# Kernel tuning notes

Hardware: AMD Instinct MI355X
Metric: run time of the kernel (lower is better)

## Reference

```python
import jax, jax.numpy as jnp
import numpy as np

DIM = 128
H = 8
HD = DIM // H
NL = 6
DFF = 2048
EPS = 1e-5
S2S_STEPS = 6


def _ln(x, g, b):
    m = jnp.mean(x, -1, keepdims=True)
    v = jnp.mean(jnp.square(x - m), -1, keepdims=True)
    return (x - m) / jnp.sqrt(v + EPS) * g + b


def _lstm_step(x, h, c, wih, whh, bih, bhh):
    # torch LSTM gate order: i, f, g, o
    gates = x @ wih.T + bih + h @ whh.T + bhh
    i, f, g, o = jnp.split(gates, 4, axis=-1)
    c = jax.nn.sigmoid(f) * c + jax.nn.sigmoid(i) * jnp.tanh(g)
    h = jax.nn.sigmoid(o) * jnp.tanh(c)
    return h, c


def setup_inputs() -> dict:
    key = jax.random.key(0)
    ks = iter(jax.random.split(key, 16))
    n = lambda shape: jax.random.normal(next(ks), shape, jnp.float32) * 0.02
    inp = {
        "data": jax.random.normal(next(ks), (64, 256, 3), jnp.float32),
        "lin0_w": n((DIM, 3)), "lin0_b": jnp.zeros((DIM,), jnp.float32),
        "attn_in_w": n((NL, 3 * DIM, DIM)), "attn_in_b": jnp.zeros((NL, 3 * DIM), jnp.float32),
        "attn_out_w": n((NL, DIM, DIM)), "attn_out_b": jnp.zeros((NL, DIM), jnp.float32),
        "ln1_g": jnp.ones((NL, DIM), jnp.float32), "ln1_b": jnp.zeros((NL, DIM), jnp.float32),
        "ff_w1": n((NL, DFF, DIM)), "ff_b1": jnp.zeros((NL, DFF), jnp.float32),
        "ff_w2": n((NL, DIM, DFF)), "ff_b2": jnp.zeros((NL, DIM), jnp.float32),
        "ln2_g": jnp.ones((NL, DIM), jnp.float32), "ln2_b": jnp.zeros((NL, DIM), jnp.float32),
        "s2s_wih": n((4 * DIM, 2 * DIM)), "s2s_whh": n((4 * DIM, DIM)),
        "s2s_bih": jnp.zeros((4 * DIM,), jnp.float32), "s2s_bhh": jnp.zeros((4 * DIM,), jnp.float32),
        "mem_wih": n((4 * DIM, 2 * DIM)), "mem_whh": n((4 * DIM, DIM)),
        "mem_bih": jnp.zeros((4 * DIM,), jnp.float32), "mem_bhh": jnp.zeros((4 * DIM,), jnp.float32),
        "lin1_w": n((DIM, DIM)), "lin1_b": jnp.zeros((DIM,), jnp.float32),
        "lin3_w": n((1, DIM)), "lin3_b": jnp.zeros((1,), jnp.float32),
    }
    return inp


def reference(data, lin0_w, lin0_b, attn_in_w, attn_in_b, attn_out_w, attn_out_b,
              ln1_g, ln1_b, ff_w1, ff_b1, ff_w2, ff_b2, ln2_g, ln2_b,
              s2s_wih, s2s_whh, s2s_bih, s2s_bhh,
              mem_wih, mem_whh, mem_bih, mem_bhh,
              lin1_w, lin1_b, lin3_w, lin3_b):
    x = jax.nn.relu(data @ lin0_w.T + lin0_b)  # [S=64, B=256, D]
    S, B, _ = x.shape
    # torch TransformerEncoder with batch_first=False: attention over axis 0,
    # axis 1 is the transformer batch. Post-norm layers (norm_first=False), relu FFN.
    for l in range(NL):
        qkv = x @ attn_in_w[l].T + attn_in_b[l]
        q, k, v = jnp.split(qkv, 3, axis=-1)
        q = q.reshape(S, B, H, HD)
        k = k.reshape(S, B, H, HD)
        v = v.reshape(S, B, H, HD)
        scores = jnp.einsum('sbhd,tbhd->bhst', q, k) / np.float32(np.sqrt(HD))
        attn = jax.nn.softmax(scores, axis=-1)
        ao = jnp.einsum('bhst,tbhd->sbhd', attn, v).reshape(S, B, DIM)
        x = _ln(x + ao @ attn_out_w[l].T + attn_out_b[l], ln1_g[l], ln1_b[l])
        ff = jax.nn.relu(x @ ff_w1[l].T + ff_b1[l]) @ ff_w2[l].T + ff_b2[l]
        x = _ln(x + ff, ln2_g[l], ln2_b[l])
    # Set2Set pooling: bidxs assign segment = axis-0 index for each block of
    # num_atoms consecutive rows of flatten(out,0,1), i.e. pool over axis 1.
    q_star = jnp.zeros((S, 2 * DIM), x.dtype)
    h = jnp.zeros((S, DIM), x.dtype)
    c = jnp.zeros((S, DIM), x.dtype)
    for _ in range(S2S_STEPS):
        h, c = _lstm_step(q_star, h, c, s2s_wih, s2s_whh, s2s_bih, s2s_bhh)
        e = jnp.einsum('bnd,bd->bn', x, h)          # [S, num_atoms]
        a = jax.nn.softmax(e, axis=-1)              # segment softmax (uniform segs)
        r = jnp.einsum('bn,bnd->bd', a, x)          # segment weighted sum
        q_star = jnp.concatenate([h, r], axis=-1)   # [S, 2D]
    # memory LSTM: seq_len 1, zero initial state (states=None branch)
    hx = jnp.zeros((S, DIM), x.dtype)
    cx = jnp.zeros((S, DIM), x.dtype)
    hx, cx = _lstm_step(q_star, hx, cx, mem_wih, mem_whh, mem_bih, mem_bhh)
    o = jax.nn.relu(hx @ lin1_w.T + lin1_b)
    v_out = (o @ lin3_w.T + lin3_b)[None]  # [1, S, 1]
    return v_out, hx[None], cx[None]
```

## Files before the change

kernel.cpp:

```cpp
#include <hip/hip_runtime.h>
#include <math.h>


typedef _Float16 __attribute__((ext_vector_type(8))) f16x8;
typedef __attribute__((ext_vector_type(4))) float f32x4;
typedef _Float16 __attribute__((ext_vector_type(2))) h16x2;

__device__ __forceinline__ unsigned short f2h(float f) {
  union { _Float16 h; unsigned short s; } x; x.h = (_Float16)f; return x.s;
}
__device__ __forceinline__ float h2f(unsigned short u) {
  union { unsigned short s; _Float16 h; } x; x.s = u; return (float)x.h;
}
__device__ __forceinline__ unsigned packh(float a, float b) {
  return (unsigned)f2h(a) | ((unsigned)f2h(b) << 16);
}
__device__ __forceinline__ uint2 pk4(float a, float b, float c, float d) {
  return make_uint2(packh(a, b), packh(c, d));
}
__device__ __forceinline__ float hlo(unsigned u) {
  union { unsigned short s; _Float16 h; } x; x.s = (unsigned short)(u & 0xffff);
  return (float)x.h;
}
__device__ __forceinline__ float hhi(unsigned u) {
  union { unsigned short s; _Float16 h; } x; x.s = (unsigned short)(u >> 16);
  return (float)x.h;
}
__device__ __forceinline__ float fdot2u(unsigned a, unsigned b, float c) {
#if __has_builtin(__builtin_amdgcn_fdot2)
  union U { unsigned u; h16x2 h; };
  U x, y; x.u = a; y.u = b;
  return __builtin_amdgcn_fdot2(x.h, y.h, c, false);
#else
  return c + hlo(a) * hlo(b) + hhi(a) * hhi(b);
#endif
}
__device__ __forceinline__ float fexp(float x) { return __expf(x); }
__device__ __forceinline__ float sigf(float x) {
  return 1.f / (1.f + __expf(-x));
}
__device__ __forceinline__ float ftanh(float x) {
  float e = __expf(2.f * x);
  return 1.f - 2.f / (e + 1.f);
}

__device__ __forceinline__ void gl2lds16(const void* g, void* l) {
  __builtin_amdgcn_global_load_lds(
      (const __attribute__((address_space(1))) unsigned int*)g,
      (__attribute__((address_space(3))) unsigned int*)l, 16, 0, 0);
}

__global__ __launch_bounds__(256) void convw_kernel(
    const float* __restrict__ aiw, const float* __restrict__ aow,
    const float* __restrict__ w1, const float* __restrict__ w2,
    const float* __restrict__ wih, const float* __restrict__ whh,
    const float* __restrict__ mwih,
    unsigned short* __restrict__ o0, unsigned short* __restrict__ o1,
    unsigned short* __restrict__ o2, unsigned short* __restrict__ o3,
    unsigned short* __restrict__ o4, unsigned short* __restrict__ o5,
    unsigned short* __restrict__ o6) {
  int i = blockIdx.x * 256 + threadIdx.x;
  if (i < 294912) {
    int l = i / 49152, o = i % 49152;
    int j = o & 7, fr = (o >> 3) & 15, fq = (o >> 7) & 3, ks = (o >> 9) & 3,
        rb = o >> 11;
    o0[i] = f2h(aiw[l * 49152 + (rb * 16 + fr) * 128 + ks * 32 + fq * 8 + j]);
  } else if (i < 393216) {
    int ii = i - 294912;
    int l = ii / 16384, o = ii % 16384;
    int j = o & 7, fr = (o >> 3) & 15, fq = (o >> 7) & 3, ks = (o >> 9) & 3,
        rb = o >> 11;
    o1[ii] = f2h(aow[l * 16384 + (rb * 16 + fr) * 128 + ks * 32 + fq * 8 + j]);
  } else if (i < 1966080) {
    int ii = i - 393216;
    int l = ii >> 18, o = ii & 262143;
    int j = o & 7, fr = (o >> 3) & 15, fq = (o >> 7) & 3, ks = (o >> 9) & 3,
        rb = o >> 11;
    o2[ii] = f2h(w1[l * 262144 + (rb * 16 + fr) * 128 + ks * 32 + fq * 8 + j]);
  } else if (i < 3538944) {
    int ii = i - 1966080;
    int l = ii >> 18, o = ii & 262143;
    int j = o & 7, fr = (o >> 3) & 15, fq = (o >> 7) & 3, ks = (o >> 9) & 63,
        rb = o >> 15;
    o3[ii] = f2h(w2[l * 262144 + (rb * 16 + fr) * 2048 + ks * 32 + fq * 8 + j]);
  } else if (i < 3670016) {
    int j = i - 3538944; o4[j] = f2h(wih[j]);
  } else if (i < 3735552) {
    int j = i - 3670016; o5[j] = f2h(whh[j]);
  } else {
    int j = i - 3735552; o6[j] = f2h(mwih[j]);
  }
}

__global__ __launch_bounds__(256) void lin0_kernel(
    const float* __restrict__ data, const float* __restrict__ w,
    const float* __restrict__ b, float* __restrict__ x,
    unsigned short* __restrict__ xb) {
  int i = blockIdx.x * 256 + threadIdx.x;
  int n = i >> 7, d = i & 127;
  float v = b[d] + data[n * 3 + 0] * w[d * 3 + 0]
                 + data[n * 3 + 1] * w[d * 3 + 1]
                 + data[n * 3 + 2] * w[d * 3 + 2];
  v = fmaxf(v, 0.0f);
  x[i] = v;
  xb[i] = f2h(v);
}

__global__ __launch_bounds__(256, 2) void layer_kernel(
    const unsigned short* __restrict__ xbg,
    const unsigned short* __restrict__ wqkv, const float* __restrict__ bqkv,
    const unsigned short* __restrict__ wout, const float* __restrict__ bout,
    const float* __restrict__ ln1g, const float* __restrict__ ln1b,
    const unsigned short* __restrict__ w1, const float* __restrict__ b1,
    const unsigned short* __restrict__ w2, const float* __restrict__ b2,
    const float* __restrict__ ln2g, const float* __restrict__ ln2b,
    float* __restrict__ xio, unsigned short* __restrict__ xbo) {
  __shared__ __align__(16) unsigned short SM[28672];
  __shared__ float psum[4][32], psq[4][32];
  __shared__ float2 stats[32];
  __shared__ __align__(16) uint4 zchunk;

  unsigned short* Xs = SM;
  unsigned short* Ks = SM + 8192;
  unsigned short* VT = SM + 16384;
  unsigned short* AOs = SM + 16384;
  unsigned short* Qs = SM + 24576;
  unsigned short* Xn = SM + 24576;

  int tid = threadIdx.x, w = tid >> 6, lane = tid & 63;
  int b = blockIdx.x >> 1, half = blockIdx.x & 1;
  int r4 = lane >> 4, cs = lane & 15;
  int fr = lane & 15, fq = lane >> 4;

  if (tid == 0) zchunk = make_uint4(0u, 0u, 0u, 0u);

#pragma unroll
  for (int i = 0; i < 4; i++) {
    int issue = w * 4 + i;
    int row = issue * 4 + r4;
    int g = cs ^ (row & 7);
    gl2lds16(xbg + (size_t)(row * 256 + b) * 128 + g * 8,
             (char*)Xs + issue * 1024);
  }
  f16x8 wq[4][2];
#pragma unroll
  for (int ks = 0; ks < 4; ks++)
#pragma unroll
    for (int ni = 0; ni < 2; ni++)
      wq[ks][ni] = *(const f16x8*)(wqkv + (size_t)(w * 2 + ni) * 2048 +
                                   ks * 512 + fq * 128 + fr * 8);
  __syncthreads();

  {
    f32x4 acc[2][2];
#pragma unroll
    for (int i = 0; i < 2; i++)
#pragma unroll
      for (int j = 0; j < 2; j++) acc[i][j] = (f32x4){0.f, 0.f, 0.f, 0.f};
#pragma unroll
    for (int ks = 0; ks < 4; ks++) {
      f16x8 bx[2];
#pragma unroll
      for (int mi2 = 0; mi2 < 2; mi2++) {
        int row = half * 32 + mi2 * 16 + fr;
        int kq = (ks * 4 + fq) ^ (row & 7);
        bx[mi2] = *(const f16x8*)(Xs + row * 128 + kq * 8);
      }
#pragma unroll
      for (int mi2 = 0; mi2 < 2; mi2++)
#pragma unroll
        for (int ni = 0; ni < 2; ni++)
          acc[mi2][ni] = __builtin_amdgcn_mfma_f32_16x16x32_f16(
              wq[ks][ni], bx[mi2], acc[mi2][ni], 0, 0, 0);
    }
#pragma unroll
    for (int ni = 0; ni < 2; ni++) {
      int fb = (w * 2 + ni) * 16 + fq * 4;
      float4 bv = *(const float4*)&bqkv[fb];
#pragma unroll
      for (int mi2 = 0; mi2 < 2; mi2++) {
        int srow = mi2 * 16 + fr;
        *(uint2*)(Qs + srow * 128 + (((fb >> 3) ^ (srow & 7)) << 3) +
                  (fb & 7)) =
            pk4(acc[mi2][ni][0] + bv.x, acc[mi2][ni][1] + bv.y,
                acc[mi2][ni][2] + bv.z, acc[mi2][ni][3] + bv.w);
      }
    }
  }
  {
    f16x8 wk[4][2];
#pragma unroll
    for (int ks = 0; ks < 4; ks++)
#pragma unroll
      for (int ni = 0; ni < 2; ni++)
        wk[ks][ni] = *(const f16x8*)(wqkv + (size_t)(8 + w * 2 + ni) * 2048 +
                                     ks * 512 + fq * 128 + fr * 8);
    f32x4 acc[4][2];
#pragma unroll
    for (int i = 0; i < 4; i++)
#pragma unroll
      for (int j = 0; j < 2; j++) acc[i][j] = (f32x4){0.f, 0.f, 0.f, 0.f};
#pragma unroll
    for (int ks = 0; ks < 4; ks++) {
      f16x8 bx[4];
#pragma unroll
      for (int mi = 0; mi < 4; mi++) {
        int row = mi * 16 + fr;
        int kq = (ks * 4 + fq) ^ (row & 7);
        bx[mi] = *(const f16x8*)(Xs + row * 128 + kq * 8);
      }
#pragma unroll
      for (int mi = 0; mi < 4; mi++)
#pragma unroll
        for (int ni = 0; ni < 2; ni++)
          acc[mi][ni] = __builtin_amdgcn_mfma_f32_16x16x32_f16(
              wk[ks][ni], bx[mi], acc[mi][ni], 0, 0, 0);
    }
#pragma unroll
    for (int ni = 0; ni < 2; ni++) {
      int fb = (w * 2 + ni) * 16 + fq * 4;
      float4 bv = *(const float4*)&bqkv[128 + fb];
#pragma unroll
      for (int mi = 0; mi < 4; mi++) {
        int srow = mi * 16 + fr;
        *(uint2*)(Ks + srow * 128 + (((fb >> 3) ^ (srow & 7)) << 3) +
                  (fb & 7)) =
            pk4(acc[mi][ni][0] + bv.x, acc[mi][ni][1] + bv.y,
                acc[mi][ni][2] + bv.z, acc[mi][ni][3] + bv.w);
      }
    }
  }
  {
    f16x8 wv[4][2];
#pragma unroll
    for (int ks = 0; ks < 4; ks++)
#pragma unroll
      for (int ni = 0; ni < 2; ni++)
        wv[ks][ni] = *(const f16x8*)(wqkv + (size_t)(16 + w * 2 + ni) * 2048 +
                                     ks * 512 + fq * 128 + fr * 8);
    f32x4 acc[4][2];
#pragma unroll
    for (int i = 0; i < 4; i++)
#pragma unroll
      for (int j = 0; j < 2; j++) acc[i][j] = (f32x4){0.f, 0.f, 0.f, 0.f};
#pragma unroll
    for (int ks = 0; ks < 4; ks++) {
      f16x8 ax[4];
#pragma unroll
      for (int mi = 0; mi < 4; mi++) {
        int row = mi * 16 + fr;
        int kq = (ks * 4 + fq) ^ (row & 7);
        ax[mi] = *(const f16x8*)(Xs + row * 128 + kq * 8);
      }
#pragma unroll
      for (int mi = 0; mi < 4; mi++)
#pragma unroll
        for (int ni = 0; ni < 2; ni++)
          acc[mi][ni] = __builtin_amdgcn_mfma_f32_16x16x32_f16(
              ax[mi], wv[ks][ni], acc[mi][ni], 0, 0, 0);
    }
#pragma unroll
    for (int ni = 0; ni < 2; ni++) {
      int feat = (w * 2 + ni) * 16 + fr;
      float bv = bqkv[256 + feat];
#pragma unroll
      for (int mi = 0; mi < 4; mi++) {
        int sb = mi * 16 + fq * 4;
        *(uint2*)(VT + feat * 64 + (((sb >> 3) ^ (feat & 7)) << 3) +
                  (sb & 7)) =
            pk4(acc[mi][ni][0] + bv, acc[mi][ni][1] + bv,
                acc[mi][ni][2] + bv, acc[mi][ni][3] + bv);
      }
    }
  }
  f16x8 wo[4][2];
#pragma unroll
  for (int ks = 0; ks < 4; ks++)
#pragma unroll
    for (int ni = 0; ni < 2; ni++)
      wo[ks][ni] = *(const f16x8*)(wout + (size_t)(w * 2 + ni) * 2048 +
                                   ks * 512 + fq * 128 + fr * 8);
  __syncthreads();

  f32x4 po[2][2];
#pragma unroll
  for (int i = 0; i < 2; i++)
#pragma unroll
    for (int j = 0; j < 2; j++) po[i][j] = (f32x4){0.f, 0.f, 0.f, 0.f};
  {
    unsigned short* Pb = Xs + w * 2048;
#pragma unroll
    for (int hi = 0; hi < 2; hi++) {
      int h = w * 2 + hi;
      f16x8 afH[2], bfH[4];
#pragma unroll
      for (int mi2 = 0; mi2 < 2; mi2++) {
        int qrow = mi2 * 16 + fr;
        const unsigned short* pa =
            (fq < 2) ? (Qs + qrow * 128 + (((h * 2 + fq) ^ (qrow & 7)) << 3))
                     : (const unsigned short*)&zchunk;
        afH[mi2] = *(const f16x8*)pa;
      }
#pragma unroll
      for (int ti = 0; ti < 4; ti++) {
        int trow = ti * 16 + fr;
        const unsigned short* pb =
            (fq < 2) ? (Ks + trow * 128 + (((h * 2 + fq) ^ (trow & 7)) << 3))
                     : (const unsigned short*)&zchunk;
        bfH[ti] = *(const f16x8*)pb;
      }
      f32x4 sc[2][4];
#pragma unroll
      for (int i = 0; i < 2; i++)
#pragma unroll
        for (int j = 0; j < 4; j++) sc[i][j] = (f32x4){0.f, 0.f, 0.f, 0.f};
#pragma unroll
      for (int mi2 = 0; mi2 < 2; mi2++)
#pragma unroll
        for (int ti = 0; ti < 4; ti++)
          sc[mi2][ti] = __builtin_amdgcn_mfma_f32_16x16x32_f16(
              afH[mi2], bfH[ti], sc[mi2][ti], 0, 0, 0);
#pragma unroll
      for (int mi2 = 0; mi2 < 2; mi2++) {
#pragma unroll
        for (int r = 0; r < 4; r++) {
          float m = -1e30f;
#pragma unroll
          for (int ti = 0; ti < 4; ti++) m = fmaxf(m, sc[mi2][ti][r]);
          m = fmaxf(m, __shfl_xor(m, 1, 64));
          m = fmaxf(m, __shfl_xor(m, 2, 64));
          m = fmaxf(m, __shfl_xor(m, 4, 64));
          m = fmaxf(m, __shfl_xor(m, 8, 64));
          m *= 0.25f;
          float ss = 0.f;
#pragma unroll
          for (int ti = 0; ti < 4; ti++) {
            float p = fexp(sc[mi2][ti][r] * 0.25f - m);
            sc[mi2][ti][r] = p;
            ss += p;
          }
          ss += __shfl_xor(ss, 1, 64);
          ss += __shfl_xor(ss, 2, 64);
          ss += __shfl_xor(ss, 4, 64);
          ss += __shfl_xor(ss, 8, 64);
          float inv = 1.f / ss;
          int prow = mi2 * 16 + fq * 4 + r;
#pragma unroll
          for (int ti = 0; ti < 4; ti++) {
            int t = ti * 16 + fr;
            Pb[prow * 64 + (((t >> 3) ^ (prow & 7)) << 3) + (t & 7)] =
                f2h(sc[mi2][ti][r] * inv);
          }
        }
      }
#pragma unroll
      for (int ks2 = 0; ks2 < 2; ks2++) {
        f16x8 bp[2], avt;
#pragma unroll
        for (int si2 = 0; si2 < 2; si2++) {
          int prow = si2 * 16 + fr;
          int kq = (ks2 * 4 + fq) ^ (prow & 7);
          bp[si2] = *(const f16x8*)(Pb + prow * 64 + kq * 8);
        }
        {
          int vrow = h * 16 + fr;
          int kq = (ks2 * 4 + fq) ^ (vrow & 7);
          avt = *(const f16x8*)(VT + vrow * 64 + kq * 8);
        }
#pragma unroll
        for (int si2 = 0; si2 < 2; si2++)
          po[hi][si2] = __builtin_amdgcn_mfma_f32_16x16x32_f16(
              avt, bp[si2], po[hi][si2], 0, 0, 0);
      }
    }
  }
  __syncthreads();
#pragma unroll
  for (int hi = 0; hi < 2; hi++) {
    int fb = (w * 2 + hi) * 16 + fq * 4;
#pragma unroll
    for (int si2 = 0; si2 < 2; si2++) {
      int srow = si2 * 16 + fr;
      *(uint2*)(AOs + srow * 128 + (((fb >> 3) ^ (srow & 7)) << 3) +
                (fb & 7)) =
          pk4(po[hi][si2][0], po[hi][si2][1], po[hi][si2][2], po[hi][si2][3]);
    }
  }
  __syncthreads();

  {
    f32x4 acc[2][2];
#pragma unroll
    for (int i = 0; i < 2; i++)
#pragma unroll
      for (int j = 0; j < 2; j++) acc[i][j] = (f32x4){0.f, 0.f, 0.f, 0.f};
#pragma unroll
    for (int ks = 0; ks < 4; ks++) {
      f16x8 bao[2];
#pragma unroll
      for (int mi2 = 0; mi2 < 2; mi2++) {
        int row = mi2 * 16 + fr;
        int kq = (ks * 4 + fq) ^ (row & 7);
        bao[mi2] = *(const f16x8*)(AOs + row * 128 + kq * 8);
      }
#pragma unroll
      for (int mi2 = 0; mi2 < 2; mi2++)
#pragma unroll
        for (int ni = 0; ni < 2; ni++)
          acc[mi2][ni] = __builtin_amdgcn_mfma_f32_16x16x32_f16(
              wo[ks][ni], bao[mi2], acc[mi2][ni], 0, 0, 0);
    }
    float v4[2][2][4];
    float psA[2] = {0.f, 0.f}, psQ[2] = {0.f, 0.f};
#pragma unroll
    for (int ni = 0; ni < 2; ni++) {
      int fb = (w * 2 + ni) * 16 + fq * 4;
      float4 bv = *(const float4*)&bout[fb];
#pragma unroll
      for (int mi2 = 0; mi2 < 2; mi2++) {
        int rowg = half * 32 + mi2 * 16 + fr;
        float4 rs = *(const float4*)&xio[(size_t)(rowg * 256 + b) * 128 + fb];
        float t0 = acc[mi2][ni][0] + bv.x + rs.x;
        float t1 = acc[mi2][ni][1] + bv.y + rs.y;
        float t2 = acc[mi2][ni][2] + bv.z + rs.z;
        float t3 = acc[mi2][ni][3] + bv.w + rs.w;
        v4[ni][mi2][0] = t0; v4[ni][mi2][1] = t1;
        v4[ni][mi2][2] = t2; v4[ni][mi2][3] = t3;
        psA[mi2] += (t0 + t1) + (t2 + t3);
        psQ[mi2] += (t0 * t0 + t1 * t1) + (t2 * t2 + t3 * t3);
      }
    }
#pragma unroll
    for (int mi2 = 0; mi2 < 2; mi2++) {
      psA[mi2] += __shfl_xor(psA[mi2], 16, 64);
      psA[mi2] += __shfl_xor(psA[mi2], 32, 64);
      psQ[mi2] += __shfl_xor(psQ[mi2], 16, 64);
      psQ[mi2] += __shfl_xor(psQ[mi2], 32, 64);
    }
    if (fq == 0) {
#pragma unroll
      for (int mi2 = 0; mi2 < 2; mi2++) {
        psum[w][mi2 * 16 + fr] = psA[mi2];
        psq[w][mi2 * 16 + fr] = psQ[mi2];
      }
    }
    __syncthreads();
    if (tid < 32) {
      float S = 0.f, Q = 0.f;
#pragma unroll
      for (int ww = 0; ww < 4; ww++) { S += psum[ww][tid]; Q += psq[ww][tid]; }
      float m = S * (1.f / 128.f);
      float var = Q * (1.f / 128.f) - m * m;
      stats[tid] = make_float2(m, rsqrtf(var + 1e-5f));
    }
    __syncthreads();
#pragma unroll
    for (int ni = 0; ni < 2; ni++) {
      int fb = (w * 2 + ni) * 16 + fq * 4;
      float4 g4 = *(const float4*)&ln1g[fb];
      float4 b4 = *(const float4*)&ln1b[fb];
#pragma unroll
      for (int mi2 = 0; mi2 < 2; mi2++) {
        int srow = mi2 * 16 + fr;
        float2 st = stats[srow];
        float y0 = (v4[ni][mi2][0] - st.x) * st.y * g4.x + b4.x;
        float y1 = (v4[ni][mi2][1] - st.x) * st.y * g4.y + b4.y;
        float y2 = (v4[ni][mi2][2] - st.x) * st.y * g4.z + b4.z;
        float y3 = (v4[ni][mi2][3] - st.x) * st.y * g4.w + b4.w;
        *(uint2*)(Xn + srow * 128 + (((fb >> 3) ^ (srow & 7)) << 3) +
                  (fb & 7)) = pk4(y0, y1, y2, y3);
      }
    }
  }
  __syncthreads();

  f16x8 xfragF[4][2];
#pragma unroll
  for (int ks = 0; ks < 4; ks++)
#pragma unroll
    for (int mi2 = 0; mi2 < 2; mi2++) {
      int rowl = mi2 * 16 + fr;
      int kq = (ks * 4 + fq) ^ (rowl & 7);
      xfragF[ks][mi2] = *(const f16x8*)(Xn + rowl * 128 + kq * 8);
    }

  f32x4 acc2[2][2];
#pragma unroll
  for (int i = 0; i < 2; i++)
#pragma unroll
    for (int j = 0; j < 2; j++) acc2[i][j] = (f32x4){0.f, 0.f, 0.f, 0.f};

  for (int c = 0; c < 8; c++) {
    unsigned short* Hcur = SM + (c & 1) * 8192;
    f16x8 aw1[4][4];
#pragma unroll
    for (int ks = 0; ks < 4; ks++)
#pragma unroll
      for (int ni = 0; ni < 4; ni++)
        aw1[ks][ni] = *(const f16x8*)(w1 + (size_t)(c * 16 + w * 4 + ni) *
                                              2048 +
                                      ks * 512 + fq * 128 + fr * 8);
    f32x4 acc1[2][4];
#pragma unroll
    for (int i = 0; i < 2; i++)
#pragma unroll
      for (int j = 0; j < 4; j++) acc1[i][j] = (f32x4){0.f, 0.f, 0.f, 0.f};
#pragma unroll
    for (int ks = 0; ks < 4; ks++)
#pragma unroll
      for (int mi2 = 0; mi2 < 2; mi2++)
#pragma unroll
        for (int ni = 0; ni < 4; ni++)
          acc1[mi2][ni] = __builtin_amdgcn_mfma_f32_16x16x32_f16(
              aw1[ks][ni], xfragF[ks][mi2], acc1[mi2][ni], 0, 0, 0);
#pragma unroll
    for (int ni = 0; ni < 4; ni++) {
      int hb = (w * 4 + ni) * 16 + fq * 4;
      float4 bv = *(const float4*)&b1[c * 256 + hb];
#pragma unroll
      for (int mi2 = 0; mi2 < 2; mi2++) {
        int srow = mi2 * 16 + fr;
        *(uint2*)(Hcur + srow * 256 + (((hb >> 3) ^ (srow & 7)) << 3) +
                  (hb & 7)) =
            pk4(fmaxf(acc1[mi2][ni][0] + bv.x, 0.f),
                fmaxf(acc1[mi2][ni][1] + bv.y, 0.f),
                fmaxf(acc1[mi2][ni][2] + bv.z, 0.f),
                fmaxf(acc1[mi2][ni][3] + bv.w, 0.f));
      }
    }
    f16x8 aw2[8][2];
#pragma unroll
    for (int ks2 = 0; ks2 < 8; ks2++)
#pragma unroll
      for (int ni = 0; ni < 2; ni++)
        aw2[ks2][ni] = *(const f16x8*)(w2 + (size_t)(w * 2 + ni) * 32768 +
                                       (c * 8 + ks2) * 512 + fq * 128 +
                                       fr * 8);
    __syncthreads();
#pragma unroll
    for (int ks2 = 0; ks2 < 8; ks2++) {
      f16x8 bh[2];
#pragma unroll
      for (int mi2 = 0; mi2 < 2; mi2++) {
        int row = mi2 * 16 + fr;
        int kq = (ks2 * 4 + fq) ^ (row & 7);
        bh[mi2] = *(const f16x8*)(Hcur + row * 256 + kq * 8);
      }
#pragma unroll
      for (int mi2 = 0; mi2 < 2; mi2++)
#pragma unroll
        for (int ni = 0; ni < 2; ni++)
          acc2[mi2][ni] = __builtin_amdgcn_mfma_f32_16x16x32_f16(
              aw2[ks2][ni], bh[mi2], acc2[mi2][ni], 0, 0, 0);
    }
  }

  {
    float v4[2][2][4];
    float psA[2] = {0.f, 0.f}, psQ[2] = {0.f, 0.f};
#pragma unroll
    for (int ni = 0; ni < 2; ni++) {
      int fb = (w * 2 + ni) * 16 + fq * 4;
      float4 bv = *(const float4*)&b2[fb];
#pragma unroll
      for (int mi2 = 0; mi2 < 2; mi2++) {
        int srow = mi2 * 16 + fr;
        uint2 rz = *(const uint2*)(Xn + srow * 128 +
                                   (((fb >> 3) ^ (srow & 7)) << 3) + (fb & 7));
        float t0 = acc2[mi2][ni][0] + bv.x + hlo(rz.x);
        float t1 = acc2[mi2][ni][1] + bv.y + hhi(rz.x);
        float t2 = acc2[mi2][ni][2] + bv.z + hlo(rz.y);
        float t3 = acc2[mi2][ni][3] + bv.w + hhi(rz.y);
        v4[ni][mi2][0] = t0; v4[ni][mi2][1] = t1;
        v4[ni][mi2][2] = t2; v4[ni][mi2][3] = t3;
        psA[mi2] += (t0 + t1) + (t2 + t3);
        psQ[mi2] += (t0 * t0 + t1 * t1) + (t2 * t2 + t3 * t3);
      }
    }
#pragma unroll
    for (int mi2 = 0; mi2 < 2; mi2++) {
      psA[mi2] += __shfl_xor(psA[mi2], 16, 64);
      psA[mi2] += __shfl_xor(psA[mi2], 32, 64);
      psQ[mi2] += __shfl_xor(psQ[mi2], 16, 64);
      psQ[mi2] += __shfl_xor(psQ[mi2], 32, 64);
    }
    if (fq == 0) {
#pragma unroll
      for (int mi2 = 0; mi2 < 2; mi2++) {
        psum[w][mi2 * 16 + fr] = psA[mi2];
        psq[w][mi2 * 16 + fr] = psQ[mi2];
      }
    }
    __syncthreads();
    if (tid < 32) {
      float S = 0.f, Q = 0.f;
#pragma unroll
      for (int ww = 0; ww < 4; ww++) { S += psum[ww][tid]; Q += psq[ww][tid]; }
      float m = S * (1.f / 128.f);
      float var = Q * (1.f / 128.f) - m * m;
      stats[tid] = make_float2(m, rsqrtf(var + 1e-5f));
    }
    __syncthreads();
#pragma unroll
    for (int ni = 0; ni < 2; ni++) {
      int fb = (w * 2 + ni) * 16 + fq * 4;
      float4 g4 = *(const float4*)&ln2g[fb];
      float4 b4 = *(const float4*)&ln2b[fb];
#pragma unroll
      for (int mi2 = 0; mi2 < 2; mi2++) {
        int srow = mi2 * 16 + fr;
        float2 st = stats[srow];
        float y0 = (v4[ni][mi2][0] - st.x) * st.y * g4.x + b4.x;
        float y1 = (v4[ni][mi2][1] - st.x) * st.y * g4.y + b4.y;
        float y2 = (v4[ni][mi2][2] - st.x) * st.y * g4.z + b4.z;
        float y3 = (v4[ni][mi2][3] - st.x) * st.y * g4.w + b4.w;
        size_t o = (size_t)((half * 32 + srow) * 256 + b) * 128 + fb;
        *(float4*)&xio[o] = make_float4(y0, y1, y2, y3);
        *(uint2*)&xbo[o] = pk4(y0, y1, y2, y3);
      }
    }
  }
}

__global__ __launch_bounds__(512, 1) void s2s_kernel(
    const unsigned short* __restrict__ xb,
    const unsigned short* __restrict__ wihh,
    const unsigned short* __restrict__ whhh,
    const float* __restrict__ bih, const float* __restrict__ bhh,
    const unsigned short* __restrict__ mwihh,
    const float* __restrict__ mbih, const float* __restrict__ mbhh,
    const float* __restrict__ l1w, const float* __restrict__ l1b,
    const float* __restrict__ l3w, const float* __restrict__ l3b,
    float* __restrict__ out) {
  __shared__ __align__(16) unsigned xl[256 * 65];
  __shared__ __align__(16) unsigned qu[128];
  __shared__ __align__(16) float cst[128];
  __shared__ __align__(16) float gates[512];
  __shared__ __align__(16) float red[256];
  __shared__ __align__(16) float aw[256];
  int s = blockIdx.x, t = threadIdx.x, lane = t & 63, w = t >> 6;

  uint4 wreg[32], ureg[16];
  {
    const uint4* wp = (const uint4*)(wihh + (size_t)t * 256);
#pragma unroll
    for (int i = 0; i < 32; i++) wreg[i] = wp[i];
    const uint4* up = (const uint4*)(whhh + (size_t)t * 128);
#pragma unroll
    for (int i = 0; i < 16; i++) ureg[i] = up[i];
  }

  const uint4* xs4 = (const uint4*)(xb + (size_t)s * 32768);
#pragma unroll
  for (int it = 0; it < 8; it++) {
    int f = it * 512 + t;
    uint4 v = xs4[f];
    int n = f >> 4, jc = (f & 15) * 4;
    unsigned* dst = xl + n * 65 + jc;
    dst[0] = v.x; dst[1] = v.y; dst[2] = v.z; dst[3] = v.w;
  }
  if (t < 128) cst[t] = 0.f;
  __syncthreads();

  const uint4* q4 = (const uint4*)qu;
  float bsum = bih[t] + bhh[t];

  for (int step = 0; step < 6; step++) {
    if (step > 0) {
      float a0 = 0.f, a1 = 0.f, a2 = 0.f, a3 = 0.f;
#pragma unroll
      for (int i = 0; i < 16; i++) {
        uint4 qv = q4[i];
        a0 = fdot2u(wreg[i].x, qv.x, a0);
        a1 = fdot2u(wreg[i].y, qv.y, a1);
        a2 = fdot2u(wreg[i].z, qv.z, a2);
        a3 = fdot2u(wreg[i].w, qv.w, a3);
        a0 = fdot2u(ureg[i].x, qv.x, a0);
        a1 = fdot2u(ureg[i].y, qv.y, a1);
        a2 = fdot2u(ureg[i].z, qv.z, a2);
        a3 = fdot2u(ureg[i].w, qv.w, a3);
      }
#pragma unroll
      for (int i = 16; i < 32; i++) {
        uint4 qv = q4[i];
        a0 = fdot2u(wreg[i].x, qv.x, a0);
        a1 = fdot2u(wreg[i].y, qv.y, a1);
        a2 = fdot2u(wreg[i].z, qv.z, a2);
        a3 = fdot2u(wreg[i].w, qv.w, a3);
      }
      gates[t] = bsum + ((a0 + a1) + (a2 + a3));
    } else {
      gates[t] = bsum;
    }
    __syncthreads();
    if (t < 128) {
      float ig = sigf(gates[t]), fg = sigf(gates[128 + t]);
      float gg = ftanh(gates[256 + t]), og = sigf(gates[384 + t]);
      float cn = fg * cst[t] + ig * gg;
      cst[t] = cn;
      float hn = og * ftanh(cn);
      float hp = __shfl_xor(hn, 1, 64);
      if ((t & 1) == 0) qu[t >> 1] = packh(hn, hp);
    }
    __syncthreads();
    if (step > 0) {
      int n = t >> 1, p = t & 1;
      const unsigned* xr = xl + n * 65 + p * 32;
      float e0 = 0.f, e1 = 0.f;
#pragma unroll 8
      for (int i = 0; i < 32; i += 2) {
        e0 = fdot2u(xr[i], qu[p * 32 + i], e0);
        e1 = fdot2u(xr[i + 1], qu[p * 32 + i + 1], e1);
      }
      float e = e0 + e1;
      e += __shfl_xor(e, 1, 64);
      if (p == 0) red[n] = e;
      __syncthreads();
      float v0 = red[lane], v1 = red[64 + lane];
      float v2 = red[128 + lane], v3 = red[192 + lane];
      float m = fmaxf(fmaxf(v0, v1), fmaxf(v2, v3));
#pragma unroll
      for (int d = 1; d < 64; d <<= 1) m = fmaxf(m, __shfl_xor(m, d, 64));
      float p0 = fexp(v0 - m), p1 = fexp(v1 - m);
      float p2 = fexp(v2 - m), p3 = fexp(v3 - m);
      float ss = p0 + p1 + p2 + p3;
#pragma unroll
      for (int d = 1; d < 64; d <<= 1) ss += __shfl_xor(ss, d, 64);
      float Sinv = 1.f / ss;
      if (w == 0) {
        aw[lane] = p0 * Sinv; aw[64 + lane] = p1 * Sinv;
        aw[128 + lane] = p2 * Sinv; aw[192 + lane] = p3 * Sinv;
      }
    } else {
      if (t < 256) aw[t] = 1.f / 256.f;
    }
    __syncthreads();
    {
      int d = t & 127, grp = t >> 7;
      const unsigned* xc = xl + grp * 64 * 65 + (d >> 1);
      int hi = d & 1;
      const float* ap = aw + grp * 64;
      float r0 = 0.f, r1 = 0.f, r2 = 0.f, r3 = 0.f;
#pragma unroll 4
      for (int n2 = 0; n2 < 64; n2 += 4) {
        unsigned u0 = xc[n2 * 65], u1 = xc[(n2 + 1) * 65];
        unsigned u2 = xc[(n2 + 2) * 65], u3 = xc[(n2 + 3) * 65];
        r0 += ap[n2] * (hi ? hhi(u0) : hlo(u0));
        r1 += ap[n2 + 1] * (hi ? hhi(u1) : hlo(u1));
        r2 += ap[n2 + 2] * (hi ? hhi(u2) : hlo(u2));
        r3 += ap[n2 + 3] * (hi ? hhi(u3) : hlo(u3));
      }
      gates[t] = (r0 + r1) + (r2 + r3);
    }
    __syncthreads();
    if (t < 128) {
      float rd = gates[t] + gates[128 + t] + gates[256 + t] + gates[384 + t];
      float rp = __shfl_xor(rd, 1, 64);
      if ((t & 1) == 0) qu[64 + (t >> 1)] = packh(rd, rp);
    }
    __syncthreads();
  }
  {
    float a0 = 0.f, a1 = 0.f, a2 = 0.f, a3 = 0.f;
    const uint4* mp = (const uint4*)(mwihh + (size_t)t * 256);
#pragma unroll 8
    for (int i = 0; i < 32; i++) {
      uint4 wv = mp[i], qv = q4[i];
      a0 = fdot2u(wv.x, qv.x, a0);
      a1 = fdot2u(wv.y, qv.y, a1);
      a2 = fdot2u(wv.z, qv.z, a2);
      a3 = fdot2u(wv.w, qv.w, a3);
    }
    gates[t] = mbih[t] + mbhh[t] + ((a0 + a1) + (a2 + a3));
  }
  __syncthreads();
  if (t < 128) {
    float ig = sigf(gates[t]);
    float gg = ftanh(gates[256 + t]);
    float og = sigf(gates[384 + t]);
    float cx = ig * gg;
    float hx = og * ftanh(cx);
    cst[t] = hx;
    out[64 + s * 128 + t] = hx;
    out[64 + 8192 + s * 128 + t] = cx;
  }
  __syncthreads();
  if (t < 128) {
    float acc = l1b[t];
    const float4* w4 = (const float4*)(l1w + (size_t)t * 128);
    const float4* h4 = (const float4*)cst;
#pragma unroll 8
    for (int k = 0; k < 32; k++) {
      float4 a = w4[k], b = h4[k];
      acc += a.x * b.x + a.y * b.y + a.z * b.z + a.w * b.w;
    }
    red[t] = fmaxf(acc, 0.f) * l3w[t];
  } else if (t < 256) {
    red[t] = 0.f;
  }
  __syncthreads();
  for (int off = 128; off; off >>= 1) {
    if (t < off) red[t] += red[t + off];
    __syncthreads();
  }
  if (t == 0) out[s] = red[0] + l3b[0];
}

extern "C" void kernel_launch(void* const* d_in, const int* in_sizes, int n_in,
                              void* d_out, int out_size, void* d_ws,
                              size_t ws_size, hipStream_t stream) {
  const float* data       = (const float*)d_in[0];
  const float* lin0_w     = (const float*)d_in[1];
  const float* lin0_b     = (const float*)d_in[2];
  const float* attn_in_w  = (const float*)d_in[3];
  const float* attn_in_b  = (const float*)d_in[4];
  const float* attn_out_w = (const float*)d_in[5];
  const float* attn_out_b = (const float*)d_in[6];
  const float* ln1_g      = (const float*)d_in[7];
  const float* ln1_b      = (const float*)d_in[8];
  const float* ff_w1      = (const float*)d_in[9];
  const float* ff_b1      = (const float*)d_in[10];
  const float* ff_w2      = (const float*)d_in[11];
  const float* ff_b2      = (const float*)d_in[12];
  const float* ln2_g      = (const float*)d_in[13];
  const float* ln2_b      = (const float*)d_in[14];
  const float* s2s_wih    = (const float*)d_in[15];
  const float* s2s_whh    = (const float*)d_in[16];
  const float* s2s_bih    = (const float*)d_in[17];
  const float* s2s_bhh    = (const float*)d_in[18];
  const float* mem_wih    = (const float*)d_in[19];
  const float* mem_bih    = (const float*)d_in[21];
  const float* mem_bhh    = (const float*)d_in[22];
  const float* lin1_w     = (const float*)d_in[23];
  const float* lin1_b     = (const float*)d_in[24];
  const float* lin3_w     = (const float*)d_in[25];
  const float* lin3_b     = (const float*)d_in[26];
  float* out = (float*)d_out;

  char* p = (char*)d_ws;
  float* x = (float*)p;                      p += (size_t)16384 * 128 * 4;
  unsigned short* xb = (unsigned short*)p;   p += (size_t)16384 * 128 * 2;
  unsigned short* wqkv = (unsigned short*)p; p += (size_t)294912 * 2;
  unsigned short* wout = (unsigned short*)p; p += (size_t)98304 * 2;
  unsigned short* w1h = (unsigned short*)p;  p += (size_t)1572864 * 2;
  unsigned short* w2h = (unsigned short*)p;  p += (size_t)1572864 * 2;
  unsigned short* wihh = (unsigned short*)p; p += (size_t)131072 * 2;
  unsigned short* whhh = (unsigned short*)p; p += (size_t)65536 * 2;
  unsigned short* mwihh = (unsigned short*)p; p += (size_t)131072 * 2;

  convw_kernel<<<15104, 256, 0, stream>>>(
      attn_in_w, attn_out_w, ff_w1, ff_w2, s2s_wih, s2s_whh, mem_wih,
      wqkv, wout, w1h, w2h, wihh, whhh, mwihh);
  lin0_kernel<<<8192, 256, 0, stream>>>(data, lin0_w, lin0_b, x, xb);

  for (int l = 0; l < 6; l++) {
    layer_kernel<<<512, 256, 0, stream>>>(
        xb, wqkv + (size_t)l * 49152, attn_in_b + l * 384,
        wout + (size_t)l * 16384, attn_out_b + l * 128,
        ln1_g + l * 128, ln1_b + l * 128,
        w1h + (size_t)l * 262144, ff_b1 + l * 2048,
        w2h + (size_t)l * 262144, ff_b2 + l * 128,
        ln2_g + l * 128, ln2_b + l * 128, x, xb);
  }

  s2s_kernel<<<64, 512, 0, stream>>>(
      xb, wihh, whhh, s2s_bih, s2s_bhh,
      mwihh, mem_bih, mem_bhh, lin1_w, lin1_b, lin3_w, lin3_b, out);
}
```

Measured before the change: 406.2 us.

## Split Set2Set LSTM work across 1024 threads and stream weights from cache

The Set2Set kernel now launches 1024 threads per block instead of 512. Each gate row's dot product is split into two halves, and the halves are summed through shared memory. The LSTM weights are no longer preloaded into registers; they are read from global memory on every step. The attention-score and weighted-sum loops are also repartitioned across the extra threads. This aims to shorten the per-step serial chain and ease register pressure, at the cost of repeated global or cache reads of the weights and extra reduction work.

```diff
diff --git a/kernel.cpp b/kernel.cpp
--- a/kernel.cpp
+++ b/kernel.cpp
@@ -622,7 +622,7 @@
   }
 }
 
-__global__ __launch_bounds__(512, 1) void s2s_kernel(
+__global__ __launch_bounds__(1024, 1) void s2s_kernel(
     const unsigned short* __restrict__ xb,
     const unsigned short* __restrict__ wihh,
     const unsigned short* __restrict__ whhh,
@@ -635,25 +635,16 @@
   __shared__ __align__(16) unsigned xl[256 * 65];
   __shared__ __align__(16) unsigned qu[128];
   __shared__ __align__(16) float cst[128];
-  __shared__ __align__(16) float gates[512];
+  __shared__ __align__(16) float gates[1024];
   __shared__ __align__(16) float red[256];
   __shared__ __align__(16) float aw[256];
   int s = blockIdx.x, t = threadIdx.x, lane = t & 63, w = t >> 6;
-
-  uint4 wreg[32], ureg[16];
-  {
-    const uint4* wp = (const uint4*)(wihh + (size_t)t * 256);
-#pragma unroll
-    for (int i = 0; i < 32; i++) wreg[i] = wp[i];
-    const uint4* up = (const uint4*)(whhh + (size_t)t * 128);
-#pragma unroll
-    for (int i = 0; i < 16; i++) ureg[i] = up[i];
-  }
+  int t0 = t & 511, hi2 = t >> 9;
 
   const uint4* xs4 = (const uint4*)(xb + (size_t)s * 32768);
 #pragma unroll
-  for (int it = 0; it < 8; it++) {
-    int f = it * 512 + t;
+  for (int it = 0; it < 4; it++) {
+    int f = it * 1024 + t;
     uint4 v = xs4[f];
     int n = f >> 4, jc = (f & 15) * 4;
     unsigned* dst = xl + n * 65 + jc;
@@ -663,30 +654,28 @@
   __syncthreads();
 
   const uint4* q4 = (const uint4*)qu;
-  float bsum = bih[t] + bhh[t];
+  float bsum = (hi2 == 0) ? (bih[t0] + bhh[t0]) : 0.f;
+  const uint4* wp = ((const uint4*)(wihh + (size_t)t0 * 256)) + hi2 * 16;
+  const uint4* up = ((const uint4*)(whhh + (size_t)t0 * 128)) + hi2 * 8;
 
   for (int step = 0; step < 6; step++) {
     if (step > 0) {
       float a0 = 0.f, a1 = 0.f, a2 = 0.f, a3 = 0.f;
 #pragma unroll
       for (int i = 0; i < 16; i++) {
-        uint4 qv = q4[i];
-        a0 = fdot2u(wreg[i].x, qv.x, a0);
-        a1 = fdot2u(wreg[i].y, qv.y, a1);
-        a2 = fdot2u(wreg[i].z, qv.z, a2);
-        a3 = fdot2u(wreg[i].w, qv.w, a3);
-        a0 = fdot2u(ureg[i].x, qv.x, a0);
-        a1 = fdot2u(ureg[i].y, qv.y, a1);
-        a2 = fdot2u(ureg[i].z, qv.z, a2);
-        a3 = fdot2u(ureg[i].w, qv.w, a3);
-      }
-#pragma unroll
-      for (int i = 16; i < 32; i++) {
-        uint4 qv = q4[i];
-        a0 = fdot2u(wreg[i].x, qv.x, a0);
-        a1 = fdot2u(wreg[i].y, qv.y, a1);
-        a2 = fdot2u(wreg[i].z, qv.z, a2);
-        a3 = fdot2u(wreg[i].w, qv.w, a3);
+        uint4 wv = wp[i], qv = q4[hi2 * 16 + i];
+        a0 = fdot2u(wv.x, qv.x, a0);
+        a1 = fdot2u(wv.y, qv.y, a1);
+        a2 = fdot2u(wv.z, qv.z, a2);
+        a3 = fdot2u(wv.w, qv.w, a3);
+      }
+#pragma unroll
+      for (int i = 0; i < 8; i++) {
+        uint4 uv = up[i], qv = q4[hi2 * 8 + i];
+        a0 = fdot2u(uv.x, qv.x, a0);
+        a1 = fdot2u(uv.y, qv.y, a1);
+        a2 = fdot2u(uv.z, qv.z, a2);
+        a3 = fdot2u(uv.w, qv.w, a3);
       }
       gates[t] = bsum + ((a0 + a1) + (a2 + a3));
     } else {
@@ -694,8 +683,12 @@
     }
     __syncthreads();
     if (t < 128) {
-      float ig = sigf(gates[t]), fg = sigf(gates[128 + t]);
-      float gg = ftanh(gates[256 + t]), og = sigf(gates[384 + t]);
+      float g0 = gates[t] + gates[512 + t];
+      float g1 = gates[128 + t] + gates[640 + t];
+      float g2 = gates[256 + t] + gates[768 + t];
+      float g3 = gates[384 + t] + gates[896 + t];
+      float ig = sigf(g0), fg = sigf(g1);
+      float gg = ftanh(g2), og = sigf(g3);
       float cn = fg * cst[t] + ig * gg;
       cst[t] = cn;
       float hn = og * ftanh(cn);
@@ -704,17 +697,18 @@
     }
     __syncthreads();
     if (step > 0) {
-      int n = t >> 1, p = t & 1;
-      const unsigned* xr = xl + n * 65 + p * 32;
+      int n = t >> 2, sub = t & 3;
+      const unsigned* xr = xl + n * 65 + sub * 16;
       float e0 = 0.f, e1 = 0.f;
-#pragma unroll 8
-      for (int i = 0; i < 32; i += 2) {
-        e0 = fdot2u(xr[i], qu[p * 32 + i], e0);
-        e1 = fdot2u(xr[i + 1], qu[p * 32 + i + 1], e1);
+#pragma unroll
+      for (int i = 0; i < 16; i += 2) {
+        e0 = fdot2u(xr[i], qu[sub * 16 + i], e0);
+        e1 = fdot2u(xr[i + 1], qu[sub * 16 + i + 1], e1);
       }
       float e = e0 + e1;
       e += __shfl_xor(e, 1, 64);
-      if (p == 0) red[n] = e;
+      e += __shfl_xor(e, 2, 64);
+      if (sub == 0) red[n] = e;
       __syncthreads();
       float v0 = red[lane], v1 = red[64 + lane];
       float v2 = red[128 + lane], v3 = red[192 + lane];
@@ -737,12 +731,12 @@
     __syncthreads();
     {
       int d = t & 127, grp = t >> 7;
-      const unsigned* xc = xl + grp * 64 * 65 + (d >> 1);
+      const unsigned* xc = xl + grp * 32 * 65 + (d >> 1);
       int hi = d & 1;
-      const float* ap = aw + grp * 64;
+      const float* ap = aw + grp * 32;
       float r0 = 0.f, r1 = 0.f, r2 = 0.f, r3 = 0.f;
 #pragma unroll 4
-      for (int n2 = 0; n2 < 64; n2 += 4) {
+      for (int n2 = 0; n2 < 32; n2 += 4) {
         unsigned u0 = xc[n2 * 65], u1 = xc[(n2 + 1) * 65];
         unsigned u2 = xc[(n2 + 2) * 65], u3 = xc[(n2 + 3) * 65];
         r0 += ap[n2] * (hi ? hhi(u0) : hlo(u0));
@@ -754,30 +748,36 @@
     }
     __syncthreads();
     if (t < 128) {
-      float rd = gates[t] + gates[128 + t] + gates[256 + t] + gates[384 + t];
+      float rd = 0.f;
+#pragma unroll
+      for (int g = 0; g < 8; g++) rd += gates[g * 128 + t];
       float rp = __shfl_xor(rd, 1, 64);
       if ((t & 1) == 0) qu[64 + (t >> 1)] = packh(rd, rp);
     }
     __syncthreads();
   }
   {
+    const uint4* mp = ((const uint4*)(mwihh + (size_t)t0 * 256)) + hi2 * 16;
     float a0 = 0.f, a1 = 0.f, a2 = 0.f, a3 = 0.f;
-    const uint4* mp = (const uint4*)(mwihh + (size_t)t * 256);
-#pragma unroll 8
-    for (int i = 0; i < 32; i++) {
-      uint4 wv = mp[i], qv = q4[i];
+#pragma unroll
+    for (int i = 0; i < 16; i++) {
+      uint4 wv = mp[i], qv = q4[hi2 * 16 + i];
       a0 = fdot2u(wv.x, qv.x, a0);
       a1 = fdot2u(wv.y, qv.y, a1);
       a2 = fdot2u(wv.z, qv.z, a2);
       a3 = fdot2u(wv.w, qv.w, a3);
     }
-    gates[t] = mbih[t] + mbhh[t] + ((a0 + a1) + (a2 + a3));
+    float mb = (hi2 == 0) ? (mbih[t0] + mbhh[t0]) : 0.f;
+    gates[t] = mb + ((a0 + a1) + (a2 + a3));
   }
   __syncthreads();
   if (t < 128) {
-    float ig = sigf(gates[t]);
-    float gg = ftanh(gates[256 + t]);
-    float og = sigf(gates[384 + t]);
+    float g0 = gates[t] + gates[512 + t];
+    float g2 = gates[256 + t] + gates[768 + t];
+    float g3 = gates[384 + t] + gates[896 + t];
+    float ig = sigf(g0);
+    float gg = ftanh(g2);
+    float og = sigf(g3);
     float cx = ig * gg;
     float hx = og * ftanh(cx);
     cst[t] = hx;
@@ -863,7 +863,7 @@
         ln2_g + l * 128, ln2_b + l * 128, x, xb);
   }
 
-  s2s_kernel<<<64, 512, 0, stream>>>(
+  s2s_kernel<<<64, 1024, 0, stream>>>(
       xb, wihh, whhh, s2s_bih, s2s_bhh,
       mwihh, mem_bih, mem_bhh, lin1_w, lin1_b, lin3_w, lin3_b, out);
 }
```

Result: slower. 454.9 us (+12.0%).
